# Performance work log

Hardware: AMD Instinct MI355X
Metric: run time of the kernel (lower is better)

The kernel has to match this reference:

```python
import jax, jax.numpy as jnp
import numpy as np

B, N, F_DIM, G_DIM, E_CAT, N_HEAD = 8, 1024, 128, 64, 2, 4
N_EDGES = 16384
L0 = 256          # NodeEmbedding hidden layer (layers=[256,128] -> last replaced by feature_size)
ALPHA = 0.5       # cfg.alpha
EPS = 1e-5        # BatchNorm eps
SLOPE = 0.01      # leaky_relu default negative slope


def _glorot(k, shape):
    stdv = float(np.sqrt(6.0 / (shape[-2] + shape[-1])))
    return jax.random.uniform(k, shape, jnp.float32, -stdv, stdv)


def setup_inputs() -> dict:
    key = jax.random.key(0)
    ks = jax.random.split(key, 8)
    X = jax.random.normal(ks[0], (B, N, F_DIM), dtype=jnp.float32)
    A = jax.random.randint(ks[1], (B, E_CAT, 2, N_EDGES), 0, N, dtype=jnp.int32)
    Ws = _glorot(ks[2], (E_CAT, N_HEAD * F_DIM, G_DIM))
    Wq = _glorot(ks[3], (E_CAT, N_HEAD * F_DIM, 1))
    Wv = _glorot(ks[4], (E_CAT, N_HEAD * F_DIM, 1))
    W_emb1 = _glorot(ks[5], (F_DIM, N_HEAD * E_CAT * G_DIM))   # Embedding1, bias=False
    W_lin0 = _glorot(ks[6], (L0, F_DIM))                        # NodeEmbedding linear0
    W_lin1 = _glorot(ks[7], (F_DIM, L0))                        # NodeEmbedding linear1
    return {"A": A, "X": X, "Ws": Ws, "Wq": Wq, "Wv": Wv,
            "W_emb1": W_emb1, "W_lin0": W_lin0, "W_lin1": W_lin1, "mini_batch": 1}


def _bn(x):
    # BatchNorm1d in training mode, affine = identity (weight=1, bias=0)
    mu = jnp.mean(x, axis=0)
    var = jnp.var(x, axis=0)  # biased variance, as torch uses for normalization
    return (x - mu) * jax.lax.rsqrt(var + EPS)


def _build_adj(A):
    # torch.sparse_coo_tensor(...).to_dense() sums duplicate edges
    adj = jnp.zeros((B, E_CAT, N, N), jnp.float32)
    b_idx = jnp.arange(B)[:, None, None]
    e_idx = jnp.arange(E_CAT)[None, :, None]
    return adj.at[b_idx, e_idx, A[:, :, 0], A[:, :, 1]].add(1.0)


def reference(A, X, Ws, Wq, Wv, W_emb1, W_lin0, W_lin1, mini_batch):
    Ws_r = Ws.reshape(E_CAT, N_HEAD, F_DIM, G_DIM)
    Wq_r = Wq.reshape(E_CAT, N_HEAD, F_DIM)   # last dim of Wq param is 1
    Wv_r = Wv.reshape(E_CAT, N_HEAD, F_DIM)

    Wh = jnp.einsum('bnf,ehfg->behng', X, Ws_r)   # [B,E,H,N,G]
    q = jnp.einsum('bnf,ehf->behn', X, Wq_r)      # [B,E,H,N]
    v = jnp.einsum('bnf,ehf->behn', X, Wv_r)

    adj = _build_adj(A)                            # [B,E,N,N]
    # e = (Wq @ Wv.T) * E, then leaky_relu and row softmax (dim=1 on [N,N] = last axis)
    scores = q[:, :, :, :, None] * v[:, :, :, None, :] * adj[:, :, None]
    scores = jnp.where(scores >= 0, scores, SLOPE * scores)
    a = jax.nn.softmax(scores, axis=-1)
    H = jnp.einsum('behnm,behmg->behng', a, Wh)    # [B,E,H,N,G]

    # concat over heads: [B,N, head-major (E*G)]
    H = H.transpose(0, 3, 2, 1, 4).reshape(B * N, N_HEAD * E_CAT * G_DIM)
    H = jax.nn.relu(H @ W_emb1.T)
    Xf = X.reshape(B * N, F_DIM)
    H = _bn((1.0 - ALPHA) * H + ALPHA * Xf)

    # NodeEmbedding: Linear -> BN -> ELU -> Linear
    Z = jax.nn.elu(_bn(H @ W_lin0.T))
    Z = Z @ W_lin1.T
    Z = _bn(H + Z)
    return Z.reshape(B, N, F_DIM)
```

## Files before the change

### kernel.cpp

```cpp
#include <hip/hip_runtime.h>
#include <hip/hip_bf16.h>

#define B_    8
#define N_    1024
#define F_    128
#define G_    64
#define EC    2
#define NHD   4
#define NE    16384
#define L0_   256
#define ALPHA_ 0.5f
#define EPS_   1e-5f
#define SLOPE_ 0.01f
#define ROWS  (B_*N_)
#define C1    (NHD*EC*G_)

typedef __attribute__((ext_vector_type(8))) short s8bf;
typedef __attribute__((ext_vector_type(4))) float f32x4;

__device__ __forceinline__ float ldv(const float* p, size_t i) { return p[i]; }
__device__ __forceinline__ float ldv(const __hip_bfloat16* p, size_t i) {
  unsigned short u = *(const unsigned short*)&p[i];
  return __uint_as_float((unsigned)u << 16);
}
__device__ __forceinline__ unsigned short f2b(float f) {
  unsigned u = __float_as_uint(f);
  u = (u + 0x7FFFu + ((u >> 16) & 1u)) >> 16;
  return (unsigned short)u;
}
__device__ __forceinline__ float b2f(unsigned short u) {
  return __uint_as_float((unsigned)u << 16);
}

__device__ __forceinline__ float wmaxf(float v) {
#pragma unroll
  for (int o = 32; o; o >>= 1) v = fmaxf(v, __shfl_xor(v, o, 64));
  return v;
}
__device__ __forceinline__ float wsumf(float v) {
#pragma unroll
  for (int o = 32; o; o >>= 1) v += __shfl_xor(v, o, 64);
  return v;
}

__global__ void k_detect(const unsigned short* Xu, int* flag) {
  int idx = blockIdx.x * 256 + threadIdx.x;
  unsigned short u = Xu[idx];
  if ((u & 0x7F80u) == 0x7F80u) atomicOr(flag, 1);
}

__device__ __forceinline__ unsigned short cvt_at(const void* p, size_t i, int isf) {
  return isf ? f2b(((const float*)p)[i]) : ((const unsigned short*)p)[i];
}
__global__ void k_cvtw(const void* X, const void* Ws, const void* We1, const void* Wl1,
                       const void* Wl0, unsigned short* Xb, unsigned short* Wsb,
                       unsigned short* We1b, unsigned short* Wl1b, unsigned short* Wl0b,
                       const int* flag) {
  int isf = *flag;
  int bid = blockIdx.x, t = threadIdx.x;
  if (bid < 4096) {
    int i = bid * 256 + t; Xb[i] = cvt_at(X, i, isf);
  } else if (bid < 4352) {
    int i = (bid - 4096) * 256 + t; We1b[i] = cvt_at(We1, i, isf);
  } else if (bid < 4480) {
    int i = (bid - 4352) * 256 + t; Wl1b[i] = cvt_at(Wl1, i, isf);
  } else if (bid < 4608) {
    int i = (bid - 4480) * 256 + t; Wl0b[i] = cvt_at(Wl0, i, isf);
  } else {
    int i = (bid - 4608) * 256 + t;
    int eh = i >> 13, rem = i & 8191;
    int g = rem >> 7, f = rem & 127;
    Wsb[eh * 8192 + g * 128 + f] = cvt_at(Ws, (size_t)eh * 8192 + f * 64 + g, isf);
  }
}

template <typename T>
__device__ __forceinline__ void proj_qv_body(const T* X, const T* Wq, const T* Wv,
                                             float* q, float* v) {
  int tid = threadIdx.x, lane = tid & 63, w = tid >> 6;
  int r = blockIdx.x * 4 + w;
  int n = r & (N_ - 1); int beh = r >> 10; int be = beh >> 2, h = beh & 3;
  int b = be >> 1, e = be & 1;
  const T* xr = X + ((size_t)(b * N_ + n)) * F_;
  const T* wq = Wq + (e * NHD + h) * F_;
  const T* wv = Wv + (e * NHD + h) * F_;
  float x0 = ldv(xr, lane), x1 = ldv(xr, lane + 64);
  float aq = x0 * ldv(wq, lane) + x1 * ldv(wq, lane + 64);
  float av = x0 * ldv(wv, lane) + x1 * ldv(wv, lane + 64);
  aq = wsumf(aq); av = wsumf(av);
  if (lane == 0) { q[r] = aq; v[r] = av; }
}
__global__ void k_proj_qv(const void* X, const void* Wq, const void* Wv,
                          float* q, float* v, const int* flag) {
  if (*flag) proj_qv_body<float>((const float*)X, (const float*)Wq, (const float*)Wv, q, v);
  else       proj_qv_body<__hip_bfloat16>((const __hip_bfloat16*)X, (const __hip_bfloat16*)Wq,
                                          (const __hip_bfloat16*)Wv, q, v);
}

template <int K>
__device__ __forceinline__ void mfma_core(const unsigned short* __restrict__ Ab,
                                          const unsigned short* __restrict__ Wb,
                                          int r0, int c0, f32x4* acc) {
  int lane = threadIdx.x & 63; int q = lane >> 4, c15 = lane & 15;
  constexpr int RS = K / 8;
  const s8bf* ap = (const s8bf*)Ab + (size_t)(r0 + c15) * RS + q;
  const s8bf* bp = (const s8bf*)Wb + (size_t)(c0 + c15) * RS + q;
#pragma unroll
  for (int ks = 0; ks < K / 32; ++ks) {
    s8bf a  = ap[ks * 4];
    s8bf b0 = bp[ks * 4];
    s8bf b1 = bp[16 * RS + ks * 4];
    s8bf b2 = bp[32 * RS + ks * 4];
    s8bf b3 = bp[48 * RS + ks * 4];
    acc[0] = __builtin_amdgcn_mfma_f32_16x16x32_bf16(a, b0, acc[0], 0, 0, 0);
    acc[1] = __builtin_amdgcn_mfma_f32_16x16x32_bf16(a, b1, acc[1], 0, 0, 0);
    acc[2] = __builtin_amdgcn_mfma_f32_16x16x32_bf16(a, b2, acc[2], 0, 0, 0);
    acc[3] = __builtin_amdgcn_mfma_f32_16x16x32_bf16(a, b3, acc[3], 0, 0, 0);
  }
}

template <int K, int MODE>
__device__ __forceinline__ void mfma_core_t(const float* __restrict__ Araw,
                                            const float* sum, const float* ssq,
                                            const unsigned short* __restrict__ Wb,
                                            int r0, int c0, f32x4* acc) {
  int lane = threadIdx.x & 63; int q = lane >> 4, c15 = lane & 15;
  constexpr int RS = K / 8;
  const float* ap = Araw + (size_t)(r0 + c15) * K + q * 8;
  const s8bf* bp = (const s8bf*)Wb + (size_t)(c0 + c15) * RS + q;
#pragma unroll
  for (int ks = 0; ks < K / 32; ++ks) {
    float av[8];
    *(float4*)&av[0] = *(const float4*)(ap + ks * 32);
    *(float4*)&av[4] = *(const float4*)(ap + ks * 32 + 4);
    s8bf a;
#pragma unroll
    for (int j = 0; j < 8; ++j) {
      int c = q * 8 + ks * 32 + j;
      float mean = sum[c] * (1.f / ROWS);
      float var = ssq[c] * (1.f / ROWS) - mean * mean;
      float y = (av[j] - mean) * rsqrtf(var + EPS_);
      if (MODE == 2) y = (y > 0.f) ? y : (expf(y) - 1.f);
      a[j] = (short)f2b(y);
    }
    s8bf b0 = bp[ks * 4];
    s8bf b1 = bp[16 * RS + ks * 4];
    s8bf b2 = bp[32 * RS + ks * 4];
    s8bf b3 = bp[48 * RS + ks * 4];
    acc[0] = __builtin_amdgcn_mfma_f32_16x16x32_bf16(a, b0, acc[0], 0, 0, 0);
    acc[1] = __builtin_amdgcn_mfma_f32_16x16x32_bf16(a, b1, acc[1], 0, 0, 0);
    acc[2] = __builtin_amdgcn_mfma_f32_16x16x32_bf16(a, b2, acc[2], 0, 0, 0);
    acc[3] = __builtin_amdgcn_mfma_f32_16x16x32_bf16(a, b3, acc[3], 0, 0, 0);
  }
}

__global__ __launch_bounds__(64) void k_whm(const unsigned short* Xb,
                                            const unsigned short* Wsb,
                                            unsigned short* Whb, float* S) {
  int r0 = blockIdx.x * 16; int eh = blockIdx.y;
  f32x4 acc[4] = {{0,0,0,0},{0,0,0,0},{0,0,0,0},{0,0,0,0}};
  mfma_core<128>(Xb, Wsb + eh * 8192, r0, 0, acc);
  int lane = threadIdx.x, q = lane >> 4, c15 = lane & 15;
  int b = r0 >> 10; int beh = b * 8 + eh;
  unsigned short* WhB = Whb + ((size_t)beh * N_ + (r0 & (N_ - 1))) * G_;
#pragma unroll
  for (int nc = 0; nc < 4; ++nc) {
    float s = 0.f;
#pragma unroll
    for (int i = 0; i < 4; ++i) {
      float o = acc[nc][i];
      WhB[(size_t)(q * 4 + i) * G_ + nc * 16 + c15] = f2b(o);
      s += o;
    }
    s += __shfl_xor(s, 16, 64); s += __shfl_xor(s, 32, 64);
    if (lane < 16) atomicAdd(&S[(size_t)beh * G_ + nc * 16 + lane], s);
  }
}

__global__ void k_scatter2(const int* A, int* fill, int* colbuf) {
  int idx = blockIdx.x * 256 + threadIdx.x;
  int be = idx >> 14, i = idx & (NE - 1);
  int row = A[(size_t)(be * 2) * NE + i];
  int col = A[(size_t)(be * 2 + 1) * NE + i];
  int p = atomicAdd(&fill[be * N_ + row], 1);
  if (p < 64) colbuf[((size_t)(be * N_ + row)) * 64 + p] = col;
}

__global__ __launch_bounds__(256) void k_attn3(const float* q, const float* v,
                                               const unsigned short* Whb,
                                               const float* S, const int* fill,
                                               const int* colbuf, unsigned short* Hcatb) {
  __shared__ int s_col[4][64];
  __shared__ int s_cnt[4][64];
  int tid = threadIdx.x, lane = tid & 63, w = tid >> 6;
  int p = blockIdx.x * 4 + w;
  int be = p >> 10, n = p & (N_ - 1);
  int b = be >> 1, e = be & 1;
  s_col[w][lane] = 0; s_cnt[w][lane] = 0;
  int L = fill[be * N_ + n];
  int Lc = (L > 64) ? 64 : L;
  int myc = (lane < Lc) ? colbuf[((size_t)(be * N_ + n)) * 64 + lane] : -1;
  int cct = 0, firstk = 64;
  for (int k = 0; k < Lc; ++k) {
    int ck = __shfl(myc, k, 64);
    if (myc >= 0 && ck == myc) { cct++; if (k < firstk) firstk = k; }
  }
  bool act = (lane < Lc) && (firstk == lane);
  unsigned long long mask = __ballot(act);
  int pos = __popcll(mask & ((1ull << lane) - 1ull));
  if (act) { s_col[w][pos] = myc; s_cnt[w][pos] = cct; }
  int Ld = __popcll(mask);
  int colc = s_col[w][lane];
  int cntc = s_cnt[w][lane];
  int eg = lane >> 4, g4 = (lane & 15) << 2;
  size_t outb = ((size_t)(b * N_ + n)) * C1 + e * G_ + g4;
  float fN = (float)(N_ - Ld);
#pragma unroll
  for (int h = 0; h < 4; ++h) {
    int beh = (be << 2) | h;
    float qn = q[beh * N_ + n];
    float sc = -1e30f;
    if (lane < Ld) {
      float t = qn * v[beh * N_ + colc] * (float)cntc;
      sc = (t >= 0.f) ? t : SLOPE_ * t;
    }
    float M = fmaxf(0.f, wmaxf(sc));
    float Ej = (lane < Ld) ? expf(sc - M) : 0.f;
    float sumE = wsumf(Ej);
    float em = expf(-M);
    float Z = fN * em + sumE;
    float wgt = (lane < Ld) ? (Ej - em) / Z : 0.f;
    float4 accv = make_float4(0.f, 0.f, 0.f, 0.f);
    if (eg == 0) {
      float4 s4 = *(const float4*)&S[(size_t)beh * G_ + g4];
      float sca = em / Z;
      accv.x = sca * s4.x; accv.y = sca * s4.y; accv.z = sca * s4.z; accv.w = sca * s4.w;
    }
    const unsigned short* WhB = Whb + (size_t)beh * N_ * G_;
    for (int k0 = 0; k0 < Ld; k0 += 4) {
      int kk = k0 + eg;
      float wk = __shfl(wgt, kk, 64);
      int ck = __shfl(colc, kk, 64);
      ushort4 xu = *(const ushort4*)&WhB[(size_t)ck * G_ + g4];
      accv.x += wk * b2f(xu.x); accv.y += wk * b2f(xu.y);
      accv.z += wk * b2f(xu.z); accv.w += wk * b2f(xu.w);
    }
    accv.x += __shfl_xor(accv.x, 16, 64); accv.y += __shfl_xor(accv.y, 16, 64);
    accv.z += __shfl_xor(accv.z, 16, 64); accv.w += __shfl_xor(accv.w, 16, 64);
    accv.x += __shfl_xor(accv.x, 32, 64); accv.y += __shfl_xor(accv.y, 32, 64);
    accv.z += __shfl_xor(accv.z, 32, 64); accv.w += __shfl_xor(accv.w, 32, 64);
    if (lane < 16) {
      ushort4 o;
      o.x = f2b(accv.x); o.y = f2b(accv.y); o.z = f2b(accv.z); o.w = f2b(accv.w);
      *(ushort4*)&Hcatb[outb + (size_t)h * (EC * G_)] = o;
    }
  }
}

template <typename TX>
__device__ __forceinline__ void mm1_ep(f32x4* acc, const TX* X, float* T4,
                                       float* sum1, float* ssq1, int r0, int c0) {
  int lane = threadIdx.x, q = lane >> 4, c15 = lane & 15;
#pragma unroll
  for (int nc = 0; nc < 4; ++nc) {
    int cc = c0 + nc * 16 + c15;
    float s = 0.f, s2 = 0.f;
#pragma unroll
    for (int i = 0; i < 4; ++i) {
      int rr = r0 + q * 4 + i;
      float o = fmaxf(acc[nc][i], 0.f);
      o = 0.5f * o + 0.5f * ldv(X, (size_t)rr * F_ + cc);
      T4[(size_t)rr * F_ + cc] = o;
      s += o; s2 += o * o;
    }
    s += __shfl_xor(s, 16, 64); s += __shfl_xor(s, 32, 64);
    s2 += __shfl_xor(s2, 16, 64); s2 += __shfl_xor(s2, 32, 64);
    if (lane < 16) {
      atomicAdd(&sum1[c0 + nc * 16 + lane], s);
      atomicAdd(&ssq1[c0 + nc * 16 + lane], s2);
    }
  }
}
__global__ __launch_bounds__(64) void k_mm1m(const unsigned short* Hcatb,
                                             const unsigned short* We1b, const void* X,
                                             float* T4, float* sum1, float* ssq1,
                                             const int* flag) {
  int r0 = blockIdx.x * 16, c0 = blockIdx.y * 64;
  f32x4 acc[4] = {{0,0,0,0},{0,0,0,0},{0,0,0,0},{0,0,0,0}};
  mfma_core<512>(Hcatb, We1b, r0, c0, acc);
  if (*flag) mm1_ep<float>(acc, (const float*)X, T4, sum1, ssq1, r0, c0);
  else       mm1_ep<__hip_bfloat16>(acc, (const __hip_bfloat16*)X, T4, sum1, ssq1, r0, c0);
}

__global__ __launch_bounds__(64) void k_lin0m(const float* T4, const float* sum1,
                                              const float* ssq1, const unsigned short* Wl0b,
                                              float* Z0, float* sum2, float* ssq2) {
  int r0 = blockIdx.x * 16, c0 = blockIdx.y * 64;
  f32x4 acc[4] = {{0,0,0,0},{0,0,0,0},{0,0,0,0},{0,0,0,0}};
  mfma_core_t<128, 1>(T4, sum1, ssq1, Wl0b, r0, c0, acc);
  int lane = threadIdx.x, q = lane >> 4, c15 = lane & 15;
#pragma unroll
  for (int nc = 0; nc < 4; ++nc) {
    int cc = c0 + nc * 16 + c15;
    float s = 0.f, s2 = 0.f;
#pragma unroll
    for (int i = 0; i < 4; ++i) {
      int rr = r0 + q * 4 + i;
      float o = acc[nc][i];
      Z0[(size_t)rr * L0_ + cc] = o;
      s += o; s2 += o * o;
    }
    s += __shfl_xor(s, 16, 64); s += __shfl_xor(s, 32, 64);
    s2 += __shfl_xor(s2, 16, 64); s2 += __shfl_xor(s2, 32, 64);
    if (lane < 16) {
      atomicAdd(&sum2[c0 + nc * 16 + lane], s);
      atomicAdd(&ssq2[c0 + nc * 16 + lane], s2);
    }
  }
}

__global__ __launch_bounds__(64) void k_lin1m(const float* Z0, const float* sum2,
                                              const float* ssq2, const unsigned short* Wl1b,
                                              const float* T4, const float* sum1,
                                              const float* ssq1,
                                              float* T6, float* sum3, float* ssq3) {
  int r0 = blockIdx.x * 16, c0 = blockIdx.y * 64;
  f32x4 acc[4] = {{0,0,0,0},{0,0,0,0},{0,0,0,0},{0,0,0,0}};
  mfma_core_t<256, 2>(Z0, sum2, ssq2, Wl1b, r0, c0, acc);
  int lane = threadIdx.x, q = lane >> 4, c15 = lane & 15;
#pragma unroll
  for (int nc = 0; nc < 4; ++nc) {
    int cc = c0 + nc * 16 + c15;
    float mean = sum1[cc] * (1.f / ROWS);
    float var = ssq1[cc] * (1.f / ROWS) - mean * mean;
    float rs = rsqrtf(var + EPS_);
    float s = 0.f, s2 = 0.f;
#pragma unroll
    for (int i = 0; i < 4; ++i) {
      int rr = r0 + q * 4 + i;
      float o = acc[nc][i] + (T4[(size_t)rr * F_ + cc] - mean) * rs;
      T6[(size_t)rr * F_ + cc] = o;
      s += o; s2 += o * o;
    }
    s += __shfl_xor(s, 16, 64); s += __shfl_xor(s, 32, 64);
    s2 += __shfl_xor(s2, 16, 64); s2 += __shfl_xor(s2, 32, 64);
    if (lane < 16) {
      atomicAdd(&sum3[c0 + nc * 16 + lane], s);
      atomicAdd(&ssq3[c0 + nc * 16 + lane], s2);
    }
  }
}

__global__ void k_norm_out(const float* in, void* out, const float* sum, const float* ssq,
                           const int* flag) {
  int idx = blockIdx.x * 256 + threadIdx.x; int c = idx & (F_ - 1);
  float mean = sum[c] * (1.f / ROWS);
  float var = ssq[c] * (1.f / ROWS) - mean * mean;
  float y = (in[idx] - mean) * rsqrtf(var + EPS_);
  if (*flag) ((float*)out)[idx] = y;
  else       ((__hip_bfloat16*)out)[idx] = __float2bfloat16(y);
}

extern "C" void kernel_launch(void* const* d_in, const int* in_sizes, int n_in,
                              void* d_out, int out_size, void* d_ws, size_t ws_size,
                              hipStream_t stream) {
  const int* A    = (const int*)d_in[0];
  const void* X   = d_in[1];
  const void* Ws  = d_in[2];
  const void* Wq  = d_in[3];
  const void* Wv  = d_in[4];
  const void* We1 = d_in[5];
  const void* Wl0 = d_in[6];
  const void* Wl1 = d_in[7];

  char* ws = (char*)d_ws;
  size_t off = 0;
  auto alloc = [&](size_t bytes) { size_t o = off; off += (bytes + 255) & ~(size_t)255; return o; };
  size_t o_fill   = alloc(16 * N_ * 4);
  size_t o_stats  = alloc(1024 * 4);
  size_t o_flag   = alloc(256);
  size_t o_S      = alloc((size_t)64 * G_ * 4);
  size_t zero_bytes = off;
  size_t o_colbuf = alloc((size_t)16 * N_ * 64 * 4);
  size_t o_q      = alloc((size_t)64 * N_ * 4);
  size_t o_v      = alloc((size_t)64 * N_ * 4);
  size_t o_Whb    = alloc((size_t)64 * N_ * G_ * 2);
  size_t o_Hcatb  = alloc((size_t)ROWS * C1 * 2);
  size_t o_T4     = alloc((size_t)ROWS * F_ * 4);
  size_t o_T6     = alloc((size_t)ROWS * F_ * 4);
  size_t o_Z0     = alloc((size_t)ROWS * L0_ * 4);
  size_t o_Xb     = alloc((size_t)ROWS * F_ * 2);
  size_t o_Wsb    = alloc((size_t)8 * G_ * F_ * 2);
  size_t o_We1b   = alloc((size_t)F_ * C1 * 2);
  size_t o_Wl1b   = alloc((size_t)F_ * L0_ * 2);
  size_t o_Wl0b   = alloc((size_t)L0_ * F_ * 2);

  int*   fill   = (int*)(ws + o_fill);
  float* stats  = (float*)(ws + o_stats);
  int*   flag   = (int*)(ws + o_flag);
  float* S      = (float*)(ws + o_S);
  int*   colbuf = (int*)(ws + o_colbuf);
  float* q      = (float*)(ws + o_q);
  float* v      = (float*)(ws + o_v);
  unsigned short* Whb   = (unsigned short*)(ws + o_Whb);
  unsigned short* Hcatb = (unsigned short*)(ws + o_Hcatb);
  float* T4     = (float*)(ws + o_T4);
  float* T6     = (float*)(ws + o_T6);
  float* Z0     = (float*)(ws + o_Z0);
  unsigned short* Xb    = (unsigned short*)(ws + o_Xb);
  unsigned short* Wsb   = (unsigned short*)(ws + o_Wsb);
  unsigned short* We1b  = (unsigned short*)(ws + o_We1b);
  unsigned short* Wl1b  = (unsigned short*)(ws + o_Wl1b);
  unsigned short* Wl0b  = (unsigned short*)(ws + o_Wl0b);
  float* sum1 = stats,       *ssq1 = stats + 128;
  float* sum2 = stats + 256, *ssq2 = stats + 512;
  float* sum3 = stats + 768, *ssq3 = stats + 896;

  hipMemsetAsync(ws, 0, zero_bytes, stream);

  k_detect<<<512, 256, 0, stream>>>((const unsigned short*)X, flag);
  k_cvtw<<<4864, 256, 0, stream>>>(X, Ws, We1, Wl1, Wl0, Xb, Wsb, We1b, Wl1b, Wl0b, flag);

  k_proj_qv<<<(64 * N_) / 4, 256, 0, stream>>>(X, Wq, Wv, q, v, flag);
  k_whm<<<dim3(ROWS / 16, 8), 64, 0, stream>>>(Xb, Wsb, Whb, S);

  k_scatter2<<<(16 * NE) / 256, 256, 0, stream>>>(A, fill, colbuf);
  k_attn3<<<(16 * N_) / 4, 256, 0, stream>>>(q, v, Whb, S, fill, colbuf, Hcatb);

  k_mm1m<<<dim3(ROWS / 16, 2), 64, 0, stream>>>(Hcatb, We1b, X, T4, sum1, ssq1, flag);
  k_lin0m<<<dim3(ROWS / 16, 4), 64, 0, stream>>>(T4, sum1, ssq1, Wl0b, Z0, sum2, ssq2);
  k_lin1m<<<dim3(ROWS / 16, 2), 64, 0, stream>>>(Z0, sum2, ssq2, Wl1b, T4, sum1, ssq1,
                                                 T6, sum3, ssq3);
  k_norm_out<<<(ROWS * F_) / 256, 256, 0, stream>>>(T6, d_out, sum3, ssq3, flag);

  (void)in_sizes; (void)n_in; (void)out_size; (void)ws_size;
}
```

Before: 236.6 us.

## Merge small prep kernels, pack 4 waves per GEMM block, remap attention blocks by XCD

The format-detect kernel and the edge scatter now run as one launch, and the weight conversion and q/v projection run as another, which cuts the number of kernel launches. The MFMA GEMM kernels now run 4 independent 64-thread waves per 256-thread block, giving a quarter as many blocks. The attention kernel maps blocks so that each XCD handles one batch's edge categories, which is meant to improve L2 locality for the Wh rows. Merging launches removes per-launch overhead, but the prep kernel's detect and scatter halves now run concurrently with each other.

```diff
diff --git a/kernel.cpp b/kernel.cpp
--- a/kernel.cpp
+++ b/kernel.cpp
@@ -43,19 +43,47 @@
   return v;
 }
 
-__global__ void k_detect(const unsigned short* Xu, int* flag) {
-  int idx = blockIdx.x * 256 + threadIdx.x;
-  unsigned short u = Xu[idx];
-  if ((u & 0x7F80u) == 0x7F80u) atomicOr(flag, 1);
+__global__ void k_prep(const unsigned short* Xu, int* flag,
+                       const int* A, int* fill, int* colbuf) {
+  int bid = blockIdx.x, tid = threadIdx.x;
+  if (bid < 512) {
+    int idx = bid * 256 + tid;
+    unsigned short u = Xu[idx];
+    if ((u & 0x7F80u) == 0x7F80u) atomicOr(flag, 1);
+  } else {
+    int idx = (bid - 512) * 256 + tid;
+    int be = idx >> 14, i = idx & (NE - 1);
+    int row = A[(size_t)(be * 2) * NE + i];
+    int col = A[(size_t)(be * 2 + 1) * NE + i];
+    int p = atomicAdd(&fill[be * N_ + row], 1);
+    if (p < 64) colbuf[((size_t)(be * N_ + row)) * 64 + p] = col;
+  }
 }
 
 __device__ __forceinline__ unsigned short cvt_at(const void* p, size_t i, int isf) {
   return isf ? f2b(((const float*)p)[i]) : ((const unsigned short*)p)[i];
 }
-__global__ void k_cvtw(const void* X, const void* Ws, const void* We1, const void* Wl1,
-                       const void* Wl0, unsigned short* Xb, unsigned short* Wsb,
-                       unsigned short* We1b, unsigned short* Wl1b, unsigned short* Wl0b,
-                       const int* flag) {
+template <typename T>
+__device__ __forceinline__ void proj_qv_body(const T* X, const T* Wq, const T* Wv,
+                                             float* q, float* v, int pb) {
+  int tid = threadIdx.x, lane = tid & 63, w = tid >> 6;
+  int r = pb * 4 + w;
+  int n = r & (N_ - 1); int beh = r >> 10; int be = beh >> 2, h = beh & 3;
+  int b = be >> 1, e = be & 1;
+  const T* xr = X + ((size_t)(b * N_ + n)) * F_;
+  const T* wq = Wq + (e * NHD + h) * F_;
+  const T* wv = Wv + (e * NHD + h) * F_;
+  float x0 = ldv(xr, lane), x1 = ldv(xr, lane + 64);
+  float aq = x0 * ldv(wq, lane) + x1 * ldv(wq, lane + 64);
+  float av = x0 * ldv(wv, lane) + x1 * ldv(wv, lane + 64);
+  aq = wsumf(aq); av = wsumf(av);
+  if (lane == 0) { q[r] = aq; v[r] = av; }
+}
+__global__ void k_cvt2(const void* X, const void* Ws, const void* We1, const void* Wl1,
+                       const void* Wl0, const void* Wq, const void* Wv,
+                       unsigned short* Xb, unsigned short* Wsb, unsigned short* We1b,
+                       unsigned short* Wl1b, unsigned short* Wl0b,
+                       float* q, float* v, const int* flag) {
   int isf = *flag;
   int bid = blockIdx.x, t = threadIdx.x;
   if (bid < 4096) {
@@ -66,35 +94,17 @@
     int i = (bid - 4352) * 256 + t; Wl1b[i] = cvt_at(Wl1, i, isf);
   } else if (bid < 4608) {
     int i = (bid - 4480) * 256 + t; Wl0b[i] = cvt_at(Wl0, i, isf);
-  } else {
+  } else if (bid < 4864) {
     int i = (bid - 4608) * 256 + t;
     int eh = i >> 13, rem = i & 8191;
     int g = rem >> 7, f = rem & 127;
     Wsb[eh * 8192 + g * 128 + f] = cvt_at(Ws, (size_t)eh * 8192 + f * 64 + g, isf);
-  }
-}
-
-template <typename T>
-__device__ __forceinline__ void proj_qv_body(const T* X, const T* Wq, const T* Wv,
-                                             float* q, float* v) {
-  int tid = threadIdx.x, lane = tid & 63, w = tid >> 6;
-  int r = blockIdx.x * 4 + w;
-  int n = r & (N_ - 1); int beh = r >> 10; int be = beh >> 2, h = beh & 3;
-  int b = be >> 1, e = be & 1;
-  const T* xr = X + ((size_t)(b * N_ + n)) * F_;
-  const T* wq = Wq + (e * NHD + h) * F_;
-  const T* wv = Wv + (e * NHD + h) * F_;
-  float x0 = ldv(xr, lane), x1 = ldv(xr, lane + 64);
-  float aq = x0 * ldv(wq, lane) + x1 * ldv(wq, lane + 64);
-  float av = x0 * ldv(wv, lane) + x1 * ldv(wv, lane + 64);
-  aq = wsumf(aq); av = wsumf(av);
-  if (lane == 0) { q[r] = aq; v[r] = av; }
-}
-__global__ void k_proj_qv(const void* X, const void* Wq, const void* Wv,
-                          float* q, float* v, const int* flag) {
-  if (*flag) proj_qv_body<float>((const float*)X, (const float*)Wq, (const float*)Wv, q, v);
-  else       proj_qv_body<__hip_bfloat16>((const __hip_bfloat16*)X, (const __hip_bfloat16*)Wq,
-                                          (const __hip_bfloat16*)Wv, q, v);
+  } else {
+    int pb = bid - 4864;
+    if (isf) proj_qv_body<float>((const float*)X, (const float*)Wq, (const float*)Wv, q, v, pb);
+    else     proj_qv_body<__hip_bfloat16>((const __hip_bfloat16*)X, (const __hip_bfloat16*)Wq,
+                                          (const __hip_bfloat16*)Wv, q, v, pb);
+  }
 }
 
 template <int K>
@@ -154,13 +164,14 @@
   }
 }
 
-__global__ __launch_bounds__(64) void k_whm(const unsigned short* Xb,
-                                            const unsigned short* Wsb,
-                                            unsigned short* Whb, float* S) {
-  int r0 = blockIdx.x * 16; int eh = blockIdx.y;
+__global__ __launch_bounds__(256) void k_whm(const unsigned short* Xb,
+                                             const unsigned short* Wsb,
+                                             unsigned short* Whb, float* S) {
+  int w = threadIdx.x >> 6;
+  int r0 = (blockIdx.x * 4 + w) * 16; int eh = blockIdx.y;
   f32x4 acc[4] = {{0,0,0,0},{0,0,0,0},{0,0,0,0},{0,0,0,0}};
   mfma_core<128>(Xb, Wsb + eh * 8192, r0, 0, acc);
-  int lane = threadIdx.x, q = lane >> 4, c15 = lane & 15;
+  int lane = threadIdx.x & 63, q = lane >> 4, c15 = lane & 15;
   int b = r0 >> 10; int beh = b * 8 + eh;
   unsigned short* WhB = Whb + ((size_t)beh * N_ + (r0 & (N_ - 1))) * G_;
 #pragma unroll
@@ -177,26 +188,15 @@
   }
 }
 
-__global__ void k_scatter2(const int* A, int* fill, int* colbuf) {
-  int idx = blockIdx.x * 256 + threadIdx.x;
-  int be = idx >> 14, i = idx & (NE - 1);
-  int row = A[(size_t)(be * 2) * NE + i];
-  int col = A[(size_t)(be * 2 + 1) * NE + i];
-  int p = atomicAdd(&fill[be * N_ + row], 1);
-  if (p < 64) colbuf[((size_t)(be * N_ + row)) * 64 + p] = col;
-}
-
 __global__ __launch_bounds__(256) void k_attn3(const float* q, const float* v,
                                                const unsigned short* Whb,
                                                const float* S, const int* fill,
                                                const int* colbuf, unsigned short* Hcatb) {
-  __shared__ int s_col[4][64];
-  __shared__ int s_cnt[4][64];
   int tid = threadIdx.x, lane = tid & 63, w = tid >> 6;
-  int p = blockIdx.x * 4 + w;
-  int be = p >> 10, n = p & (N_ - 1);
+  int xcd = blockIdx.x & 7, j = blockIdx.x >> 3;
+  int be = (xcd << 1) | (j & 1);
+  int n = (j >> 1) * 4 + w;
   int b = be >> 1, e = be & 1;
-  s_col[w][lane] = 0; s_cnt[w][lane] = 0;
   int L = fill[be * N_ + n];
   int Lc = (L > 64) ? 64 : L;
   int myc = (lane < Lc) ? colbuf[((size_t)(be * N_ + n)) * 64 + lane] : -1;
@@ -208,6 +208,9 @@
   bool act = (lane < Lc) && (firstk == lane);
   unsigned long long mask = __ballot(act);
   int pos = __popcll(mask & ((1ull << lane) - 1ull));
+  __shared__ int s_col[4][64];
+  __shared__ int s_cnt[4][64];
+  s_col[w][lane] = 0; s_cnt[w][lane] = 0;
   if (act) { s_col[w][pos] = myc; s_cnt[w][pos] = cct; }
   int Ld = __popcll(mask);
   int colc = s_col[w][lane];
@@ -260,7 +263,7 @@
 template <typename TX>
 __device__ __forceinline__ void mm1_ep(f32x4* acc, const TX* X, float* T4,
                                        float* sum1, float* ssq1, int r0, int c0) {
-  int lane = threadIdx.x, q = lane >> 4, c15 = lane & 15;
+  int lane = threadIdx.x & 63, q = lane >> 4, c15 = lane & 15;
 #pragma unroll
   for (int nc = 0; nc < 4; ++nc) {
     int cc = c0 + nc * 16 + c15;
@@ -281,24 +284,26 @@
     }
   }
 }
-__global__ __launch_bounds__(64) void k_mm1m(const unsigned short* Hcatb,
-                                             const unsigned short* We1b, const void* X,
-                                             float* T4, float* sum1, float* ssq1,
-                                             const int* flag) {
-  int r0 = blockIdx.x * 16, c0 = blockIdx.y * 64;
+__global__ __launch_bounds__(256) void k_mm1m(const unsigned short* Hcatb,
+                                              const unsigned short* We1b, const void* X,
+                                              float* T4, float* sum1, float* ssq1,
+                                              const int* flag) {
+  int w = threadIdx.x >> 6;
+  int r0 = (blockIdx.x * 4 + w) * 16, c0 = blockIdx.y * 64;
   f32x4 acc[4] = {{0,0,0,0},{0,0,0,0},{0,0,0,0},{0,0,0,0}};
   mfma_core<512>(Hcatb, We1b, r0, c0, acc);
   if (*flag) mm1_ep<float>(acc, (const float*)X, T4, sum1, ssq1, r0, c0);
   else       mm1_ep<__hip_bfloat16>(acc, (const __hip_bfloat16*)X, T4, sum1, ssq1, r0, c0);
 }
 
-__global__ __launch_bounds__(64) void k_lin0m(const float* T4, const float* sum1,
-                                              const float* ssq1, const unsigned short* Wl0b,
-                                              float* Z0, float* sum2, float* ssq2) {
-  int r0 = blockIdx.x * 16, c0 = blockIdx.y * 64;
+__global__ __launch_bounds__(256) void k_lin0m(const float* T4, const float* sum1,
+                                               const float* ssq1, const unsigned short* Wl0b,
+                                               float* Z0, float* sum2, float* ssq2) {
+  int w = threadIdx.x >> 6;
+  int r0 = (blockIdx.x * 4 + w) * 16, c0 = blockIdx.y * 64;
   f32x4 acc[4] = {{0,0,0,0},{0,0,0,0},{0,0,0,0},{0,0,0,0}};
   mfma_core_t<128, 1>(T4, sum1, ssq1, Wl0b, r0, c0, acc);
-  int lane = threadIdx.x, q = lane >> 4, c15 = lane & 15;
+  int lane = threadIdx.x & 63, q = lane >> 4, c15 = lane & 15;
 #pragma unroll
   for (int nc = 0; nc < 4; ++nc) {
     int cc = c0 + nc * 16 + c15;
@@ -319,15 +324,16 @@
   }
 }
 
-__global__ __launch_bounds__(64) void k_lin1m(const float* Z0, const float* sum2,
-                                              const float* ssq2, const unsigned short* Wl1b,
-                                              const float* T4, const float* sum1,
-                                              const float* ssq1,
-                                              float* T6, float* sum3, float* ssq3) {
-  int r0 = blockIdx.x * 16, c0 = blockIdx.y * 64;
+__global__ __launch_bounds__(256) void k_lin1m(const float* Z0, const float* sum2,
+                                               const float* ssq2, const unsigned short* Wl1b,
+                                               const float* T4, const float* sum1,
+                                               const float* ssq1,
+                                               float* T6, float* sum3, float* ssq3) {
+  int w = threadIdx.x >> 6;
+  int r0 = (blockIdx.x * 4 + w) * 16, c0 = blockIdx.y * 64;
   f32x4 acc[4] = {{0,0,0,0},{0,0,0,0},{0,0,0,0},{0,0,0,0}};
   mfma_core_t<256, 2>(Z0, sum2, ssq2, Wl1b, r0, c0, acc);
-  int lane = threadIdx.x, q = lane >> 4, c15 = lane & 15;
+  int lane = threadIdx.x & 63, q = lane >> 4, c15 = lane & 15;
 #pragma unroll
   for (int nc = 0; nc < 4; ++nc) {
     int cc = c0 + nc * 16 + c15;
@@ -418,19 +424,15 @@
 
   hipMemsetAsync(ws, 0, zero_bytes, stream);
 
-  k_detect<<<512, 256, 0, stream>>>((const unsigned short*)X, flag);
-  k_cvtw<<<4864, 256, 0, stream>>>(X, Ws, We1, Wl1, Wl0, Xb, Wsb, We1b, Wl1b, Wl0b, flag);
-
-  k_proj_qv<<<(64 * N_) / 4, 256, 0, stream>>>(X, Wq, Wv, q, v, flag);
-  k_whm<<<dim3(ROWS / 16, 8), 64, 0, stream>>>(Xb, Wsb, Whb, S);
-
-  k_scatter2<<<(16 * NE) / 256, 256, 0, stream>>>(A, fill, colbuf);
+  k_prep<<<1536, 256, 0, stream>>>((const unsigned short*)X, flag, A, fill, colbuf);
+  k_cvt2<<<4864 + 16384, 256, 0, stream>>>(X, Ws, We1, Wl1, Wl0, Wq, Wv,
+                                           Xb, Wsb, We1b, Wl1b, Wl0b, q, v, flag);
+  k_whm<<<dim3(ROWS / 64, 8), 256, 0, stream>>>(Xb, Wsb, Whb, S);
   k_attn3<<<(16 * N_) / 4, 256, 0, stream>>>(q, v, Whb, S, fill, colbuf, Hcatb);
-
-  k_mm1m<<<dim3(ROWS / 16, 2), 64, 0, stream>>>(Hcatb, We1b, X, T4, sum1, ssq1, flag);
-  k_lin0m<<<dim3(ROWS / 16, 4), 64, 0, stream>>>(T4, sum1, ssq1, Wl0b, Z0, sum2, ssq2);
-  k_lin1m<<<dim3(ROWS / 16, 2), 64, 0, stream>>>(Z0, sum2, ssq2, Wl1b, T4, sum1, ssq1,
-                                                 T6, sum3, ssq3);
+  k_mm1m<<<dim3(ROWS / 64, 2), 256, 0, stream>>>(Hcatb, We1b, X, T4, sum1, ssq1, flag);
+  k_lin0m<<<dim3(ROWS / 64, 4), 256, 0, stream>>>(T4, sum1, ssq1, Wl0b, Z0, sum2, ssq2);
+  k_lin1m<<<dim3(ROWS / 64, 2), 256, 0, stream>>>(Z0, sum2, ssq2, Wl1b, T4, sum1, ssq1,
+                                                  T6, sum3, ssq3);
   k_norm_out<<<(ROWS * F_) / 256, 256, 0, stream>>>(T6, d_out, sum3, ssq3, flag);
 
   (void)in_sizes; (void)n_in; (void)out_size; (void)ws_size;
```

New measurement: 225.9 us. 4.5% less time.
